# Performance work log

Measured on AMD Instinct MI355X. Metric: run time of the kernel, lower is better.

Reference implementation:

```python
import jax, jax.numpy as jnp
import numpy as np

B, S, H, D, OUT = 4, 2048, 16, 64, 1024


def setup_inputs() -> dict:
    root = jax.random.key(0)
    ks = jax.random.split(root, 7)
    scale = 0.02
    return {
        "query": jax.random.normal(ks[0], (B, S, D), dtype=jnp.float32),
        "key": jax.random.normal(ks[1], (B, S, D), dtype=jnp.float32),
        "value": jax.random.normal(ks[2], (B, S, D), dtype=jnp.float32),
        # per-head projection weights, torch Linear layout [out, in] stacked over heads
        "Wq": jax.random.normal(ks[3], (H, D, D), dtype=jnp.float32) * scale,
        "Wk": jax.random.normal(ks[4], (H, D, D), dtype=jnp.float32) * scale,
        "Wv": jax.random.normal(ks[5], (H, D, D), dtype=jnp.float32) * scale,
        # output projection weight [output_dim, H*D]
        "Wo": jax.random.normal(ks[6], (OUT, H * D), dtype=jnp.float32) * scale,
    }


def reference(query, key, value, Wq, Wk, Wv, Wo):
    b, s, d = query.shape
    h = Wq.shape[0]
    # per-head linear projections (x @ W_h.T), batched over all heads at once
    q = jnp.einsum('bsd,hed->bhse', query, Wq)   # [B,H,S,D]
    k = jnp.einsum('bsd,hed->bhse', key, Wk)
    v = jnp.einsum('bsd,hed->bhse', value, Wv)
    scores = jnp.einsum('bhqe,bhke->bhqk', q, k) / jnp.sqrt(jnp.asarray(d, q.dtype))
    attn = jax.nn.softmax(scores, axis=-1)       # [B,H,S,S]
    o = jnp.einsum('bhqk,bhke->bhqe', attn, v)   # [B,H,S,D]
    # concat heads along feature dim -> [B,S,H*D]
    x = o.transpose(0, 2, 1, 3).reshape(b, s, h * d)
    return x @ Wo.T                               # [B,S,OUT]
```

## Files before the change

kernel.cpp:

```cpp
#include <hip/hip_runtime.h>
#include <hip/hip_bf16.h>
#include <cstdint>


#define QSCALE 0.1803368801111204f

typedef __attribute__((ext_vector_type(8))) short bf16x8;
typedef __attribute__((ext_vector_type(4))) short bf16x4;
typedef __attribute__((ext_vector_type(4))) float f32x4;
typedef __attribute__((ext_vector_type(16))) float f32x16;

typedef __attribute__((address_space(1))) unsigned int g_u32;
typedef __attribute__((address_space(3))) unsigned int l_u32;

__device__ inline unsigned short f2bf(float f) {
    union { float f; unsigned u; } v;
    v.f = f;
    unsigned r = v.u + 0x7fffu + ((v.u >> 16) & 1u);
    return (unsigned short)(r >> 16);
}

__device__ inline unsigned cvt_pk_bf16(float a, float b) {
    unsigned r;
    asm("v_cvt_pk_bf16_f32 %0, %1, %2" : "=v"(r) : "v"(a), "v"(b));
    return r;
}

__device__ inline f32x4 mfma16(bf16x8 a, bf16x8 b, f32x4 c) {
    return __builtin_amdgcn_mfma_f32_16x16x32_bf16(a, b, c, 0, 0, 0);
}
__device__ inline f32x16 mfma32(bf16x8 a, bf16x8 b, f32x16 c) {
    return __builtin_amdgcn_mfma_f32_32x32x16_bf16(a, b, c, 0, 0, 0);
}

__device__ inline float sum16(const f32x16& v) {
    float a0 = v[0] + v[1], a1 = v[2] + v[3], a2 = v[4] + v[5], a3 = v[6] + v[7];
    float a4 = v[8] + v[9], a5 = v[10] + v[11], a6 = v[12] + v[13], a7 = v[14] + v[15];
    float b0 = a0 + a1, b1 = a2 + a3, b2 = a4 + a5, b3 = a6 + a7;
    return (b0 + b1) + (b2 + b3);
}

__global__ __launch_bounds__(256) void conv_bf16(
    const float* __restrict__ q, const float* __restrict__ k, const float* __restrict__ v,
    const float* __restrict__ wq, const float* __restrict__ wk, const float* __restrict__ wv,
    const float* __restrict__ wo,
    unsigned short* __restrict__ qb, unsigned short* __restrict__ kb,
    unsigned short* __restrict__ vb,
    unsigned short* __restrict__ wqb, unsigned short* __restrict__ wkb,
    unsigned short* __restrict__ wvb, unsigned short* __restrict__ wob) {
    const int z = blockIdx.y;
    const float* src; unsigned short* dst; int n;
    switch (z) {
        case 0: src = q;  dst = qb;  n = 524288;  break;
        case 1: src = k;  dst = kb;  n = 524288;  break;
        case 2: src = v;  dst = vb;  n = 524288;  break;
        case 3: src = wq; dst = wqb; n = 65536;   break;
        case 4: src = wk; dst = wkb; n = 65536;   break;
        case 5: src = wv; dst = wvb; n = 65536;   break;
        default: src = wo; dst = wob; n = 1048576; break;
    }
    int i = (blockIdx.x * 256 + threadIdx.x) * 8;
    if (i >= n) return;
    float4 f0 = *reinterpret_cast<const float4*>(src + i);
    float4 f1 = *reinterpret_cast<const float4*>(src + i + 4);
    bf16x8 h;
    h[0] = (short)f2bf(f0.x); h[1] = (short)f2bf(f0.y);
    h[2] = (short)f2bf(f0.z); h[3] = (short)f2bf(f0.w);
    h[4] = (short)f2bf(f1.x); h[5] = (short)f2bf(f1.y);
    h[6] = (short)f2bf(f1.z); h[7] = (short)f2bf(f1.w);
    *reinterpret_cast<bf16x8*>(dst + i) = h;
}

__global__ __launch_bounds__(256) void qkv_proj(
    const unsigned short* __restrict__ qb, const unsigned short* __restrict__ kb,
    const unsigned short* __restrict__ vb,
    const unsigned short* __restrict__ wqb, const unsigned short* __restrict__ wkb,
    const unsigned short* __restrict__ wvb,
    unsigned short* __restrict__ Qp, unsigned short* __restrict__ Kp,
    unsigned short* __restrict__ Vt) {
    const int z = blockIdx.z;
    const unsigned short* X = (z == 0) ? qb : (z == 1) ? kb : vb;
    const unsigned short* W = (z == 0) ? wqb : (z == 1) ? wkb : wvb;
    const int bh = blockIdx.y;
    const int b = bh >> 4, h = bh & 15;
    const int s0 = blockIdx.x * 64;
    const int t = threadIdx.x;
    const int w = t >> 6, l = t & 63, lr = l & 15, lg = l >> 4;

    __shared__ unsigned short Xs[64][72];
    __shared__ unsigned short Ws[64][72];

    {
        const unsigned short* xsrc = X + (size_t)(b * 2048 + s0) * 64;
        const unsigned short* wsrc = W + h * 4096;
#pragma unroll
        for (int i = 0; i < 2; ++i) {
            int idx = t + i * 256;
            int r = idx >> 3, c8 = (idx & 7) * 8;
            *reinterpret_cast<bf16x8*>(&Xs[r][c8]) =
                *reinterpret_cast<const bf16x8*>(xsrc + (size_t)r * 64 + c8);
            *reinterpret_cast<bf16x8*>(&Ws[r][c8]) =
                *reinterpret_cast<const bf16x8*>(wsrc + r * 64 + c8);
        }
    }
    __syncthreads();

    f32x4 acc[4];
#pragma unroll
    for (int nt = 0; nt < 4; ++nt) acc[nt] = f32x4{0.f, 0.f, 0.f, 0.f};

    const size_t bhS = (size_t)bh * 2048 * 64;
    if (z < 2) {
#pragma unroll
        for (int kk = 0; kk < 2; ++kk) {
            bf16x8 a = *reinterpret_cast<const bf16x8*>(&Xs[w * 16 + lr][kk * 32 + lg * 8]);
#pragma unroll
            for (int nt = 0; nt < 4; ++nt) {
                bf16x8 bb = *reinterpret_cast<const bf16x8*>(&Ws[nt * 16 + lr][kk * 32 + lg * 8]);
                acc[nt] = mfma16(bb, a, acc[nt]);
            }
        }
        unsigned short* Out = (z == 0) ? Qp : Kp;
        const float scale = (z == 0) ? QSCALE : 1.0f;
        const int s = s0 + w * 16 + lr;
#pragma unroll
        for (int nt = 0; nt < 4; ++nt) {
            bf16x4 pk;
#pragma unroll
            for (int j = 0; j < 4; ++j) pk[j] = (short)f2bf(acc[nt][j] * scale);
            *reinterpret_cast<bf16x4*>(&Out[bhS + (size_t)s * 64 + nt * 16 + lg * 4]) = pk;
        }
    } else {
#pragma unroll
        for (int kk = 0; kk < 2; ++kk) {
            bf16x8 a = *reinterpret_cast<const bf16x8*>(&Xs[w * 16 + lr][kk * 32 + lg * 8]);
#pragma unroll
            for (int nt = 0; nt < 4; ++nt) {
                bf16x8 bb = *reinterpret_cast<const bf16x8*>(&Ws[nt * 16 + lr][kk * 32 + lg * 8]);
                acc[nt] = mfma16(a, bb, acc[nt]);
            }
        }
#pragma unroll
        for (int nt = 0; nt < 4; ++nt) {
            int e = nt * 16 + lr;
            int s = s0 + w * 16 + lg * 4;
            bf16x4 pk;
#pragma unroll
            for (int j = 0; j < 4; ++j) pk[j] = (short)f2bf(acc[nt][j]);
            *reinterpret_cast<bf16x4*>(&Vt[(size_t)bh * 64 * 2048 + (size_t)e * 2048 + s]) = pk;
        }
    }
}

__global__ __launch_bounds__(256, 3) void attn_kernel(
    const unsigned short* __restrict__ Qp, const unsigned short* __restrict__ Kp,
    const unsigned short* __restrict__ Vt, unsigned short* __restrict__ Xb) {
    const int bh = blockIdx.y;
    const int b = bh >> 4, h = bh & 15;
    const int t = threadIdx.x;
    const int w = t >> 6, l = t & 63;
    const int lo = l & 31, hi = l >> 5;
    const int qw = blockIdx.x * 128 + w * 32;

    __shared__ unsigned short Kbuf[2][4096];
    __shared__ unsigned short Vbuf[2][4096];

    bf16x8 bq[4];
    {
        const unsigned short* qptr = Qp + ((size_t)bh * 2048 + qw + lo) * 64 + hi * 8;
#pragma unroll
        for (int ds = 0; ds < 4; ++ds)
            bq[ds] = *reinterpret_cast<const bf16x8*>(qptr + ds * 16);
    }

    f32x16 oacc0, oacc1;
#pragma unroll
    for (int r = 0; r < 16; ++r) { oacc0[r] = 0.f; oacc1[r] = 0.f; }
    float lsum = 0.f;

    const unsigned short* kbase = Kp + (size_t)bh * 2048 * 64;
    const unsigned short* vbase = Vt + (size_t)bh * 64 * 2048;

    const int rr = l >> 3;
    const int sp = (l & 7) ^ rr;
    const int rb = w * 16;

#pragma unroll
    for (int i = 0; i < 2; ++i) {
        int r = rb + i * 8 + rr;
        __builtin_amdgcn_global_load_lds(
            (const g_u32*)(kbase + (size_t)r * 64 + sp * 8),
            (l_u32*)(&Kbuf[0][(rb + i * 8) * 64]), 16, 0, 0);
        __builtin_amdgcn_global_load_lds(
            (const g_u32*)(vbase + (size_t)r * 2048 + sp * 8),
            (l_u32*)(&Vbuf[0][(rb + i * 8) * 64]), 16, 0, 0);
    }
    __syncthreads();

    const int swz = (lo & 7) << 4;

    for (int kt = 0; kt < 32; ++kt) {
        const int cur = kt & 1;
        if (kt < 31) {
#pragma unroll
            for (int i = 0; i < 2; ++i) {
                int r = rb + i * 8 + rr;
                __builtin_amdgcn_global_load_lds(
                    (const g_u32*)(kbase + (size_t)((kt + 1) * 64 + r) * 64 + sp * 8),
                    (l_u32*)(&Kbuf[cur ^ 1][(rb + i * 8) * 64]), 16, 0, 0);
                __builtin_amdgcn_global_load_lds(
                    (const g_u32*)(vbase + (size_t)r * 2048 + (kt + 1) * 64 + sp * 8),
                    (l_u32*)(&Vbuf[cur ^ 1][(rb + i * 8) * 64]), 16, 0, 0);
            }
        }

        const char* kb = (const char*)Kbuf[cur];
        const char* vb = (const char*)Vbuf[cur];

#pragma unroll
        for (int half = 0; half < 2; ++half) {
            f32x16 s;
#pragma unroll
            for (int r = 0; r < 16; ++r) s[r] = 0.f;
            const char* krow = kb + (lo + 32 * half) * 128;
            __builtin_amdgcn_s_setprio(1);
#pragma unroll
            for (int ds = 0; ds < 4; ++ds) {
                bf16x8 ka = *reinterpret_cast<const bf16x8*>(krow + ((32 * ds + 16 * hi) ^ swz));
                s = mfma32(ka, bq[ds], s);
            }
            __builtin_amdgcn_s_setprio(0);

#pragma unroll
            for (int r = 0; r < 16; ++r) s[r] = __builtin_amdgcn_exp2f(s[r]);
            lsum += sum16(s);

#pragma unroll
            for (int ks2 = 0; ks2 < 2; ++ks2) {
                const int bb = ks2 * 8;
                unsigned w0 = cvt_pk_bf16(s[bb + 0], s[bb + 1]);
                unsigned w1 = cvt_pk_bf16(s[bb + 2], s[bb + 3]);
                unsigned w2 = cvt_pk_bf16(s[bb + 4], s[bb + 5]);
                unsigned w3 = cvt_pk_bf16(s[bb + 6], s[bb + 7]);
                asm("v_permlane32_swap_b32 %0, %1" : "+v"(w0), "+v"(w2));
                asm("v_permlane32_swap_b32 %0, %1" : "+v"(w1), "+v"(w3));
                union { unsigned u[4]; bf16x8 v; } pa;
                pa.u[0] = w0; pa.u[1] = w1; pa.u[2] = w2; pa.u[3] = w3;
                int c = (32 * (half * 2 + ks2) + 16 * hi) ^ swz;
                bf16x8 v0 = *reinterpret_cast<const bf16x8*>(vb + lo * 128 + c);
                bf16x8 v1 = *reinterpret_cast<const bf16x8*>(vb + (lo + 32) * 128 + c);
                __builtin_amdgcn_s_setprio(1);
                oacc0 = mfma32(pa.v, v0, oacc0);
                oacc1 = mfma32(pa.v, v1, oacc1);
                __builtin_amdgcn_s_setprio(0);
            }
        }
        __syncthreads();
    }

    lsum += __shfl_xor(lsum, 32);
    const size_t rowbase = (size_t)b * 2048 * 1024 + (size_t)h * 64;
#pragma unroll
    for (int r = 0; r < 16; ++r) {
        int ql = (r & 3) + 8 * (r >> 2) + 4 * hi;
        float inv = 1.0f / __shfl(lsum, ql);
        unsigned short* dst = Xb + rowbase + (size_t)(qw + ql) * 1024;
        dst[lo] = f2bf(oacc0[r] * inv);
        dst[lo + 32] = f2bf(oacc1[r] * inv);
    }
}

__global__ __launch_bounds__(256) void out_gemm(
    const unsigned short* __restrict__ Xb, const unsigned short* __restrict__ Wob,
    float* __restrict__ out) {
    const int nb = blockIdx.x * 128;
    const int mb = blockIdx.y * 128;
    const int t = threadIdx.x;
    const int w = t >> 6, l = t & 63, lr = l & 15, lg = l >> 4;
    const int wr = (w >> 1) * 64, wc = (w & 1) * 64;

    __shared__ unsigned short As[2][128 * 64];
    __shared__ unsigned short Bs[2][128 * 64];

    f32x4 acc[4][4];
#pragma unroll
    for (int mi = 0; mi < 4; ++mi)
#pragma unroll
        for (int ni = 0; ni < 4; ++ni) acc[mi][ni] = f32x4{0.f, 0.f, 0.f, 0.f};

    const int rr = l >> 3;
    const int sp = (l & 7) ^ rr;
    const int swz = (lr & 7) << 4;

#pragma unroll
    for (int i = 0; i < 4; ++i) {
        int r = w * 32 + i * 8 + rr;
        __builtin_amdgcn_global_load_lds(
            (const g_u32*)(Xb + (size_t)(mb + r) * 1024 + sp * 8),
            (l_u32*)(&As[0][(w * 32 + i * 8) * 64]), 16, 0, 0);
        __builtin_amdgcn_global_load_lds(
            (const g_u32*)(Wob + (size_t)(nb + r) * 1024 + sp * 8),
            (l_u32*)(&Bs[0][(w * 32 + i * 8) * 64]), 16, 0, 0);
    }
    __syncthreads();

    for (int kt = 0; kt < 16; ++kt) {
        const int cur = kt & 1;
        if (kt < 15) {
#pragma unroll
            for (int i = 0; i < 4; ++i) {
                int r = w * 32 + i * 8 + rr;
                __builtin_amdgcn_global_load_lds(
                    (const g_u32*)(Xb + (size_t)(mb + r) * 1024 + (kt + 1) * 64 + sp * 8),
                    (l_u32*)(&As[cur ^ 1][(w * 32 + i * 8) * 64]), 16, 0, 0);
                __builtin_amdgcn_global_load_lds(
                    (const g_u32*)(Wob + (size_t)(nb + r) * 1024 + (kt + 1) * 64 + sp * 8),
                    (l_u32*)(&Bs[cur ^ 1][(w * 32 + i * 8) * 64]), 16, 0, 0);
            }
        }

        const char* ab = (const char*)As[cur];
        const char* bbp = (const char*)Bs[cur];
#pragma unroll
        for (int kk = 0; kk < 2; ++kk) {
            const int cb = (kk * 64 + lg * 16) ^ swz;
            bf16x8 af[4], bf[4];
#pragma unroll
            for (int mi = 0; mi < 4; ++mi)
                af[mi] = *reinterpret_cast<const bf16x8*>(ab + (wr + mi * 16 + lr) * 128 + cb);
#pragma unroll
            for (int ni = 0; ni < 4; ++ni)
                bf[ni] = *reinterpret_cast<const bf16x8*>(bbp + (wc + ni * 16 + lr) * 128 + cb);
            __builtin_amdgcn_s_setprio(1);
#pragma unroll
            for (int mi = 0; mi < 4; ++mi)
#pragma unroll
                for (int ni = 0; ni < 4; ++ni)
                    acc[mi][ni] = mfma16(bf[ni], af[mi], acc[mi][ni]);
            __builtin_amdgcn_s_setprio(0);
        }
        __syncthreads();
    }

#pragma unroll
    for (int mi = 0; mi < 4; ++mi) {
        const size_t row = (size_t)(mb + wr + mi * 16 + lr);
#pragma unroll
        for (int ni = 0; ni < 4; ++ni) {
            float4 o;
            o.x = acc[mi][ni][0]; o.y = acc[mi][ni][1];
            o.z = acc[mi][ni][2]; o.w = acc[mi][ni][3];
            *reinterpret_cast<float4*>(&out[row * 1024 + nb + wc + ni * 16 + lg * 4]) = o;
        }
    }
}

extern "C" void kernel_launch(void* const* d_in, const int* in_sizes, int n_in,
                              void* d_out, int out_size, void* d_ws, size_t ws_size,
                              hipStream_t stream) {
    (void)in_sizes; (void)n_in; (void)out_size; (void)ws_size;
    const float* query = (const float*)d_in[0];
    const float* key   = (const float*)d_in[1];
    const float* value = (const float*)d_in[2];
    const float* Wq = (const float*)d_in[3];
    const float* Wk = (const float*)d_in[4];
    const float* Wv = (const float*)d_in[5];
    const float* Wo = (const float*)d_in[6];
    float* out = (float*)d_out;

    char* ws = (char*)d_ws;
    unsigned short* Qp  = (unsigned short*)(ws);
    unsigned short* Kp  = (unsigned short*)(ws + (size_t)16 * 1024 * 1024);
    unsigned short* Vt  = (unsigned short*)(ws + (size_t)32 * 1024 * 1024);
    unsigned short* Xb  = (unsigned short*)(ws + (size_t)48 * 1024 * 1024);
    unsigned short* qb  = Xb;
    unsigned short* kb  = (unsigned short*)(ws + (size_t)49 * 1024 * 1024);
    unsigned short* vb  = (unsigned short*)(ws + (size_t)50 * 1024 * 1024);
    unsigned short* Wob = (unsigned short*)(ws + (size_t)64 * 1024 * 1024);
    unsigned short* Wqb = (unsigned short*)(ws + (size_t)66 * 1024 * 1024);
    unsigned short* Wkb = Wqb + 65536;
    unsigned short* Wvb = Wkb + 65536;

    hipLaunchKernelGGL(conv_bf16, dim3(512, 7), dim3(256), 0, stream,
                       query, key, value, Wq, Wk, Wv, Wo,
                       qb, kb, vb, Wqb, Wkb, Wvb, Wob);
    hipLaunchKernelGGL(qkv_proj, dim3(32, 64, 3), dim3(256), 0, stream,
                       qb, kb, vb, Wqb, Wkb, Wvb, Qp, Kp, Vt);
    hipLaunchKernelGGL(attn_kernel, dim3(16, 64), dim3(256), 0, stream,
                       Qp, Kp, Vt, Xb);
    hipLaunchKernelGGL(out_gemm, dim3(8, 64), dim3(256), 0, stream,
                       Xb, Wob, out);
}
```

Baseline: 203.4 us.

## Fuse fp32-to-bf16 conversion into QKV projection and remap attention/GEMM block order

Removes the separate conversion pass for query/key/value and per-head weights: qkv_proj now loads fp32 directly and packs to bf16 with the hardware cvt_pk instruction while staging to LDS. Only Wo is still converted by a small standalone kernel. Software rounding is replaced everywhere by v_cvt_pk_bf16_f32, and the row sum is reduced with packed f32x2 adds. Attention blocks are renumbered so the same head is spread across blocks with occupancy hint raised to 4, and out_gemm blocks are remapped per XCD for L2 locality. qkv_proj now reads each fp32 input redundantly across 16 heads, doubling its global read bytes per block versus bf16.

```diff
diff --git a/kernel.cpp b/kernel.cpp
--- a/kernel.cpp
+++ b/kernel.cpp
@@ -7,18 +7,12 @@
 
 typedef __attribute__((ext_vector_type(8))) short bf16x8;
 typedef __attribute__((ext_vector_type(4))) short bf16x4;
+typedef __attribute__((ext_vector_type(2))) float f32x2;
 typedef __attribute__((ext_vector_type(4))) float f32x4;
 typedef __attribute__((ext_vector_type(16))) float f32x16;
 
 typedef __attribute__((address_space(1))) unsigned int g_u32;
 typedef __attribute__((address_space(3))) unsigned int l_u32;
-
-__device__ inline unsigned short f2bf(float f) {
-    union { float f; unsigned u; } v;
-    v.f = f;
-    unsigned r = v.u + 0x7fffu + ((v.u >> 16) & 1u);
-    return (unsigned short)(r >> 16);
-}
 
 __device__ inline unsigned cvt_pk_bf16(float a, float b) {
     unsigned r;
@@ -26,6 +20,14 @@
     return r;
 }
 
+__device__ inline unsigned short f2bf1(float x) {
+    return (unsigned short)cvt_pk_bf16(x, x);
+}
+
+__device__ inline uint2 pack4(float a, float b, float c, float d) {
+    uint2 u; u.x = cvt_pk_bf16(a, b); u.y = cvt_pk_bf16(c, d); return u;
+}
+
 __device__ inline f32x4 mfma16(bf16x8 a, bf16x8 b, f32x4 c) {
     return __builtin_amdgcn_mfma_f32_16x16x32_bf16(a, b, c, 0, 0, 0);
 }
@@ -33,54 +35,35 @@
     return __builtin_amdgcn_mfma_f32_32x32x16_bf16(a, b, c, 0, 0, 0);
 }
 
-__device__ inline float sum16(const f32x16& v) {
-    float a0 = v[0] + v[1], a1 = v[2] + v[3], a2 = v[4] + v[5], a3 = v[6] + v[7];
-    float a4 = v[8] + v[9], a5 = v[10] + v[11], a6 = v[12] + v[13], a7 = v[14] + v[15];
-    float b0 = a0 + a1, b1 = a2 + a3, b2 = a4 + a5, b3 = a6 + a7;
-    return (b0 + b1) + (b2 + b3);
-}
-
-__global__ __launch_bounds__(256) void conv_bf16(
-    const float* __restrict__ q, const float* __restrict__ k, const float* __restrict__ v,
-    const float* __restrict__ wq, const float* __restrict__ wk, const float* __restrict__ wv,
-    const float* __restrict__ wo,
-    unsigned short* __restrict__ qb, unsigned short* __restrict__ kb,
-    unsigned short* __restrict__ vb,
-    unsigned short* __restrict__ wqb, unsigned short* __restrict__ wkb,
-    unsigned short* __restrict__ wvb, unsigned short* __restrict__ wob) {
-    const int z = blockIdx.y;
-    const float* src; unsigned short* dst; int n;
-    switch (z) {
-        case 0: src = q;  dst = qb;  n = 524288;  break;
-        case 1: src = k;  dst = kb;  n = 524288;  break;
-        case 2: src = v;  dst = vb;  n = 524288;  break;
-        case 3: src = wq; dst = wqb; n = 65536;   break;
-        case 4: src = wk; dst = wkb; n = 65536;   break;
-        case 5: src = wv; dst = wvb; n = 65536;   break;
-        default: src = wo; dst = wob; n = 1048576; break;
-    }
+__device__ inline float sum16v(const f32x16& v) {
+    const f32x2* p = reinterpret_cast<const f32x2*>(&v);
+    f32x2 q0 = p[0] + p[1], q1 = p[2] + p[3], q2 = p[4] + p[5], q3 = p[6] + p[7];
+    f32x2 r0 = q0 + q1, r1 = q2 + q3;
+    f32x2 t = r0 + r1;
+    return t[0] + t[1];
+}
+
+__global__ __launch_bounds__(256) void wo_conv(const float* __restrict__ Wo,
+                                               unsigned short* __restrict__ Wob) {
     int i = (blockIdx.x * 256 + threadIdx.x) * 8;
-    if (i >= n) return;
-    float4 f0 = *reinterpret_cast<const float4*>(src + i);
-    float4 f1 = *reinterpret_cast<const float4*>(src + i + 4);
-    bf16x8 h;
-    h[0] = (short)f2bf(f0.x); h[1] = (short)f2bf(f0.y);
-    h[2] = (short)f2bf(f0.z); h[3] = (short)f2bf(f0.w);
-    h[4] = (short)f2bf(f1.x); h[5] = (short)f2bf(f1.y);
-    h[6] = (short)f2bf(f1.z); h[7] = (short)f2bf(f1.w);
-    *reinterpret_cast<bf16x8*>(dst + i) = h;
+    float4 f0 = *reinterpret_cast<const float4*>(Wo + i);
+    float4 f1 = *reinterpret_cast<const float4*>(Wo + i + 4);
+    uint4 h;
+    h.x = cvt_pk_bf16(f0.x, f0.y); h.y = cvt_pk_bf16(f0.z, f0.w);
+    h.z = cvt_pk_bf16(f1.x, f1.y); h.w = cvt_pk_bf16(f1.z, f1.w);
+    *reinterpret_cast<uint4*>(Wob + i) = h;
 }
 
 __global__ __launch_bounds__(256) void qkv_proj(
-    const unsigned short* __restrict__ qb, const unsigned short* __restrict__ kb,
-    const unsigned short* __restrict__ vb,
-    const unsigned short* __restrict__ wqb, const unsigned short* __restrict__ wkb,
-    const unsigned short* __restrict__ wvb,
+    const float* __restrict__ q_in, const float* __restrict__ k_in,
+    const float* __restrict__ v_in,
+    const float* __restrict__ Wq, const float* __restrict__ Wk,
+    const float* __restrict__ Wv,
     unsigned short* __restrict__ Qp, unsigned short* __restrict__ Kp,
     unsigned short* __restrict__ Vt) {
     const int z = blockIdx.z;
-    const unsigned short* X = (z == 0) ? qb : (z == 1) ? kb : vb;
-    const unsigned short* W = (z == 0) ? wqb : (z == 1) ? wkb : wvb;
+    const float* X = (z == 0) ? q_in : (z == 1) ? k_in : v_in;
+    const float* W = (z == 0) ? Wq : (z == 1) ? Wk : Wv;
     const int bh = blockIdx.y;
     const int b = bh >> 4, h = bh & 15;
     const int s0 = blockIdx.x * 64;
@@ -91,16 +74,16 @@
     __shared__ unsigned short Ws[64][72];
 
     {
-        const unsigned short* xsrc = X + (size_t)(b * 2048 + s0) * 64;
-        const unsigned short* wsrc = W + h * 4096;
-#pragma unroll
-        for (int i = 0; i < 2; ++i) {
+        const float* src = X + (size_t)(b * 2048 + s0) * 64;
+        const float* wsrc = W + (size_t)h * 4096;
+#pragma unroll
+        for (int i = 0; i < 4; ++i) {
             int idx = t + i * 256;
-            int r = idx >> 3, c8 = (idx & 7) * 8;
-            *reinterpret_cast<bf16x8*>(&Xs[r][c8]) =
-                *reinterpret_cast<const bf16x8*>(xsrc + (size_t)r * 64 + c8);
-            *reinterpret_cast<bf16x8*>(&Ws[r][c8]) =
-                *reinterpret_cast<const bf16x8*>(wsrc + r * 64 + c8);
+            int r = idx >> 4, c4 = (idx & 15) * 4;
+            float4 f = *reinterpret_cast<const float4*>(src + r * 64 + c4);
+            *reinterpret_cast<uint2*>(&Xs[r][c4]) = pack4(f.x, f.y, f.z, f.w);
+            float4 g = *reinterpret_cast<const float4*>(wsrc + r * 64 + c4);
+            *reinterpret_cast<uint2*>(&Ws[r][c4]) = pack4(g.x, g.y, g.z, g.w);
         }
     }
     __syncthreads();
@@ -125,10 +108,9 @@
         const int s = s0 + w * 16 + lr;
 #pragma unroll
         for (int nt = 0; nt < 4; ++nt) {
-            bf16x4 pk;
-#pragma unroll
-            for (int j = 0; j < 4; ++j) pk[j] = (short)f2bf(acc[nt][j] * scale);
-            *reinterpret_cast<bf16x4*>(&Out[bhS + (size_t)s * 64 + nt * 16 + lg * 4]) = pk;
+            *reinterpret_cast<uint2*>(&Out[bhS + (size_t)s * 64 + nt * 16 + lg * 4]) =
+                pack4(acc[nt][0] * scale, acc[nt][1] * scale,
+                      acc[nt][2] * scale, acc[nt][3] * scale);
         }
     } else {
 #pragma unroll
@@ -144,23 +126,23 @@
         for (int nt = 0; nt < 4; ++nt) {
             int e = nt * 16 + lr;
             int s = s0 + w * 16 + lg * 4;
-            bf16x4 pk;
-#pragma unroll
-            for (int j = 0; j < 4; ++j) pk[j] = (short)f2bf(acc[nt][j]);
-            *reinterpret_cast<bf16x4*>(&Vt[(size_t)bh * 64 * 2048 + (size_t)e * 2048 + s]) = pk;
-        }
-    }
-}
-
-__global__ __launch_bounds__(256, 3) void attn_kernel(
+            *reinterpret_cast<uint2*>(&Vt[(size_t)bh * 64 * 2048 + (size_t)e * 2048 + s]) =
+                pack4(acc[nt][0], acc[nt][1], acc[nt][2], acc[nt][3]);
+        }
+    }
+}
+
+__global__ __launch_bounds__(256, 4) void attn_kernel(
     const unsigned short* __restrict__ Qp, const unsigned short* __restrict__ Kp,
     const unsigned short* __restrict__ Vt, unsigned short* __restrict__ Xb) {
-    const int bh = blockIdx.y;
+    const int id = blockIdx.x + 16 * blockIdx.y;
+    const int bh = id & 63;
+    const int qx = id >> 6;
     const int b = bh >> 4, h = bh & 15;
     const int t = threadIdx.x;
     const int w = t >> 6, l = t & 63;
     const int lo = l & 31, hi = l >> 5;
-    const int qw = blockIdx.x * 128 + w * 32;
+    const int qw = qx * 128 + w * 32;
 
     __shared__ unsigned short Kbuf[2][4096];
     __shared__ unsigned short Vbuf[2][4096];
@@ -233,7 +215,7 @@
 
 #pragma unroll
             for (int r = 0; r < 16; ++r) s[r] = __builtin_amdgcn_exp2f(s[r]);
-            lsum += sum16(s);
+            lsum += sum16v(s);
 
 #pragma unroll
             for (int ks2 = 0; ks2 < 2; ++ks2) {
@@ -265,16 +247,18 @@
         int ql = (r & 3) + 8 * (r >> 2) + 4 * hi;
         float inv = 1.0f / __shfl(lsum, ql);
         unsigned short* dst = Xb + rowbase + (size_t)(qw + ql) * 1024;
-        dst[lo] = f2bf(oacc0[r] * inv);
-        dst[lo + 32] = f2bf(oacc1[r] * inv);
+        dst[lo] = f2bf1(oacc0[r] * inv);
+        dst[lo + 32] = f2bf1(oacc1[r] * inv);
     }
 }
 
 __global__ __launch_bounds__(256) void out_gemm(
     const unsigned short* __restrict__ Xb, const unsigned short* __restrict__ Wob,
     float* __restrict__ out) {
-    const int nb = blockIdx.x * 128;
-    const int mb = blockIdx.y * 128;
+    const int wg = blockIdx.x + 8 * blockIdx.y;
+    const int xcd = wg & 7, k2 = wg >> 3;
+    const int mb = (xcd * 8 + (k2 & 7)) * 128;
+    const int nb = (k2 >> 3) * 128;
     const int t = threadIdx.x;
     const int w = t >> 6, l = t & 63, lr = l & 15, lg = l >> 4;
     const int wr = (w >> 1) * 64, wc = (w & 1) * 64;
@@ -373,19 +357,11 @@
     unsigned short* Kp  = (unsigned short*)(ws + (size_t)16 * 1024 * 1024);
     unsigned short* Vt  = (unsigned short*)(ws + (size_t)32 * 1024 * 1024);
     unsigned short* Xb  = (unsigned short*)(ws + (size_t)48 * 1024 * 1024);
-    unsigned short* qb  = Xb;
-    unsigned short* kb  = (unsigned short*)(ws + (size_t)49 * 1024 * 1024);
-    unsigned short* vb  = (unsigned short*)(ws + (size_t)50 * 1024 * 1024);
     unsigned short* Wob = (unsigned short*)(ws + (size_t)64 * 1024 * 1024);
-    unsigned short* Wqb = (unsigned short*)(ws + (size_t)66 * 1024 * 1024);
-    unsigned short* Wkb = Wqb + 65536;
-    unsigned short* Wvb = Wkb + 65536;
-
-    hipLaunchKernelGGL(conv_bf16, dim3(512, 7), dim3(256), 0, stream,
-                       query, key, value, Wq, Wk, Wv, Wo,
-                       qb, kb, vb, Wqb, Wkb, Wvb, Wob);
+
+    hipLaunchKernelGGL(wo_conv, dim3(512), dim3(256), 0, stream, Wo, Wob);
     hipLaunchKernelGGL(qkv_proj, dim3(32, 64, 3), dim3(256), 0, stream,
-                       qb, kb, vb, Wqb, Wkb, Wvb, Qp, Kp, Vt);
+                       query, key, value, Wq, Wk, Wv, Qp, Kp, Vt);
     hipLaunchKernelGGL(attn_kernel, dim3(16, 64), dim3(256), 0, stream,
                        Qp, Kp, Vt, Xb);
     hipLaunchKernelGGL(out_gemm, dim3(8, 64), dim3(256), 0, stream,
```

After: 202.1 us. No clear change (-0.6%).
